# Performance work log

Measured on AMD Instinct MI355X. Metric: run time of the kernel, lower is better.

Reference implementation:

```python
import jax, jax.numpy as jnp
import numpy as np

NC, NK, K, PAD, SCALE, MID = 3, 64, 3, 1, 4, 4
K2, S2 = K * K, SCALE * SCALE
B, H, W = 4, 128, 128


def conv2d(x, w, b, pad):
    y = jax.lax.conv_general_dilated(x, w, (1, 1), [(pad, pad), (pad, pad)],
                                     dimension_numbers=('NCHW', 'OIHW', 'NCHW'))
    return y + b[None, :, None, None]


def bilinear_gather(x, py, px):
    # x: [B,C,H,W]; py/px: [B,K2,H,W] absolute (fractional) sample coords; zero outside.
    b, c, h, w = x.shape
    y0, x0 = jnp.floor(py), jnp.floor(px)
    wy, wx = py - y0, px - x0
    xf = x.reshape(b, c, h * w)

    def g(yi, xi):
        valid = ((yi >= 0) & (yi <= h - 1) & (xi >= 0) & (xi <= w - 1)).astype(x.dtype)
        yc = jnp.clip(yi, 0, h - 1).astype(jnp.int32)
        xc = jnp.clip(xi, 0, w - 1).astype(jnp.int32)
        idx = (yc * w + xc).reshape(b, -1)
        v = jax.vmap(lambda a, i: a[:, i])(xf, idx).reshape(b, c, *yi.shape[1:])
        return v * valid[:, None]

    return (((1 - wy) * (1 - wx))[:, None] * g(y0, x0)
            + ((1 - wy) * wx)[:, None] * g(y0, x0 + 1)
            + (wy * (1 - wx))[:, None] * g(y0 + 1, x0)
            + (wy * wx)[:, None] * g(y0 + 1, x0 + 1))


def deform_conv(x, ow, ob, mw, mb, w, b):
    # DCNv2: offsets [B,2*K2,H,W] (y,x interleaved per tap), modulation mask 2*sigmoid.
    bsz, c, h, ww = x.shape
    off = conv2d(x, ow, ob, PAD).reshape(bsz, K2, 2, h, ww)
    mask = 2.0 * jax.nn.sigmoid(conv2d(x, mw, mb, PAD))  # [B,K2,H,W]
    ky, kx = jnp.meshgrid(jnp.arange(K), jnp.arange(K), indexing='ij')
    py = jnp.arange(h)[None, None, :, None] + (ky.reshape(K2) - PAD)[None, :, None, None] + off[:, :, 0]
    px = jnp.arange(ww)[None, None, None, :] + (kx.reshape(K2) - PAD)[None, :, None, None] + off[:, :, 1]
    patches = bilinear_gather(x, py, px) * mask[:, None]  # [B,C,K2,H,W]
    return jnp.einsum('bckhw,ock->bohw', patches, w.reshape(w.shape[0], c, K2)) + b[None, :, None, None]


def convlstm(x, h, c, w, b):
    g = conv2d(jnp.concatenate([x, h], 1), w, b, PAD)
    i, f, o, gg = jnp.split(g, 4, axis=1)
    c = jax.nn.sigmoid(f) * c + jax.nn.sigmoid(i) * jnp.tanh(gg)
    return jax.nn.sigmoid(o) * jnp.tanh(c), c


def ddf_up(x, sp_w, sp_b, ch_w1, ch_b1, ch_w2, ch_b2):
    # DDFUpPack: S2 branches, per-pixel spatial filter + SE-style per-channel filter,
    # 'add' combine, per-branch dynamic KxK filtering, then pixel_shuffle(SCALE).
    bsz, c, h, w = x.shape
    sp = conv2d(x, sp_w.reshape(S2 * K2, c, K, K), sp_b.reshape(S2 * K2), PAD).reshape(bsz, S2, K2, h, w)
    pooled = x.mean((2, 3))  # global avg pool -> [B,C]
    h1 = jax.nn.relu(jnp.einsum('bc,smc->bsm', pooled, ch_w1) + ch_b1[None])
    ch = (jnp.einsum('bsm,skm->bsk', h1, ch_w2) + ch_b2[None]).reshape(bsz, S2, c, K2)
    xp = jnp.pad(x, ((0, 0), (0, 0), (PAD, PAD), (PAD, PAD)))
    patches = jnp.stack([xp[:, :, i:i + h, j:j + w] for i in range(K) for j in range(K)], 2)  # [B,C,K2,H,W]
    filt = ch[:, :, :, :, None, None] + sp[:, :, None]  # [B,S2,C,K2,H,W]
    out = jnp.einsum('bckhw,bsckhw->bcshw', patches, filt)  # [B,C,S2,H,W]
    out = out.reshape(bsz, c, SCALE, SCALE, h, w).transpose(0, 1, 4, 2, 5, 3)
    return out.reshape(bsz, c, h * SCALE, w * SCALE)  # pixel_shuffle


def _forward(X, lstm_w, lstm_b,
             d1_ow, d1_ob, d1_mw, d1_mb, d1_w, d1_b,
             d2_ow, d2_ob, d2_mw, d2_mb, d2_w, d2_b,
             d3_ow, d3_ob, d3_mw, d3_mb, d3_w, d3_b,
             conv_w, conv_b, sp_w, sp_b, ch_w1, ch_b1, ch_w2, ch_b2):
    lr = X
    bsz, _, h, w = X.shape
    z = jnp.zeros((bsz, NK, h, w), X.dtype)
    hid, cell = convlstm(X, z, z, lstm_w, lstm_b)
    x = deform_conv(jnp.concatenate([hid, lr], 1), d1_ow, d1_ob, d1_mw, d1_mb, d1_w, d1_b)
    x = deform_conv(jnp.concatenate([x, lr], 1), d2_ow, d2_ob, d2_mw, d2_mb, d2_w, d2_b)
    x = deform_conv(jnp.concatenate([x, lr], 1), d3_ow, d3_ob, d3_mw, d3_mb, d3_w, d3_b)
    x = conv2d(jnp.concatenate([x, lr], 1), conv_w, conv_b, PAD)
    out = jnp.clip(ddf_up(x, sp_w, sp_b, ch_w1, ch_b1, ch_w2, ch_b2), 0.0, 255.0)
    return out, hid, cell


def setup_inputs():
    key = jax.random.key(0)
    ks = iter(jax.random.split(key, 40))

    def p(shape, s=0.05):
        return jax.random.normal(next(ks), shape, jnp.float32) * s

    cin = NK + NC
    d = {'X': jax.random.normal(next(ks), (B, NC, H, W), jnp.float32),
         'lstm_w': p((4 * NK, NC + NK, K, K)), 'lstm_b': p((4 * NK,))}
    for i in (1, 2, 3):
        d[f'd{i}_ow'] = p((2 * K2, cin, K, K)); d[f'd{i}_ob'] = p((2 * K2,))
        d[f'd{i}_mw'] = p((K2, cin, K, K));     d[f'd{i}_mb'] = p((K2,))
        d[f'd{i}_w'] = p((NK, cin, K, K));      d[f'd{i}_b'] = p((NK,))
    d['conv_w'] = p((NC, cin, K, K)); d['conv_b'] = p((NC,))
    d['sp_w'] = p((S2, K2, NC, K, K)); d['sp_b'] = p((S2, K2))
    d['ch_w1'] = p((S2, MID, NC)); d['ch_b1'] = p((S2, MID))
    d['ch_w2'] = p((S2, NC * K2, MID)); d['ch_b2'] = p((S2, NC * K2))
    return d


def reference(X, lstm_w, lstm_b,
              d1_ow, d1_ob, d1_mw, d1_mb, d1_w, d1_b,
              d2_ow, d2_ob, d2_mw, d2_mb, d2_w, d2_b,
              d3_ow, d3_ob, d3_mw, d3_mb, d3_w, d3_b,
              conv_w, conv_b, sp_w, sp_b, ch_w1, ch_b1, ch_w2, ch_b2):
    return _forward(X, lstm_w, lstm_b,
                    d1_ow, d1_ob, d1_mw, d1_mb, d1_w, d1_b,
                    d2_ow, d2_ob, d2_mw, d2_mb, d2_w, d2_b,
                    d3_ow, d3_ob, d3_mw, d3_mb, d3_w, d3_b,
                    conv_w, conv_b, sp_w, sp_b, ch_w1, ch_b1, ch_w2, ch_b2)
```

## Files before the change

### kernel.cpp

```cpp
#include <hip/hip_runtime.h>
#include <hip/hip_bf16.h>
#include <math.h>

#define NC 3
#define NK 64
#define KK 3
#define K2 9
#define PAD 1
#define SCALE 4
#define S2 16
#define MID 4
#define B 4
#define H 128
#define W 128
#define HW (H*W)
#define CIN 67
#define OUT_HW (H*SCALE)
#define CST 64
#define NSTRIPE 64

typedef short bf16x8 __attribute__((ext_vector_type(8)));
typedef float f32x4 __attribute__((ext_vector_type(4)));
typedef float f32x2 __attribute__((ext_vector_type(2)));
typedef unsigned int u32x4 __attribute__((ext_vector_type(4)));
typedef unsigned int u32x2 __attribute__((ext_vector_type(2)));

__device__ __forceinline__ float fast_sigmoid(float v) { return 1.f / (1.f + __expf(-v)); }
__device__ __forceinline__ float fast_tanh(float v) { return 2.f / (1.f + __expf(-2.f * v)) - 1.f; }

__device__ __forceinline__ unsigned short f2bf(float f) {
    unsigned int u = __float_as_uint(f);
    unsigned int r = (u + 0x7FFFu + ((u >> 16) & 1u)) >> 16;
    return (unsigned short)r;
}

__device__ __forceinline__ f32x2 unpk(unsigned int u) {
    f32x2 r;
    r[0] = __uint_as_float(u << 16);
    r[1] = __uint_as_float(u & 0xffff0000u);
    return r;
}

__device__ __forceinline__ void load_patch(const float* __restrict__ xc, int y, int x, float* p) {
#pragma unroll
    for (int dy = -1; dy <= 1; dy++) {
#pragma unroll
        for (int dx = -1; dx <= 1; dx++) {
            int yy = y + dy, xx = x + dx;
            float v = (yy >= 0 && yy < H && xx >= 0 && xx < W) ? xc[yy * W + xx] : 0.f;
            p[(dy + 1) * 3 + (dx + 1)] = v;
        }
    }
}

__global__ void k_prep(const float* __restrict__ lw,
                       const float* __restrict__ dw0, const float* __restrict__ dw1,
                       const float* __restrict__ dw2,
                       const float* __restrict__ ow0, const float* __restrict__ ow1,
                       const float* __restrict__ ow2,
                       const float* __restrict__ mw0, const float* __restrict__ mw1,
                       const float* __restrict__ mw2,
                       unsigned short* __restrict__ aplk,
                       unsigned short* __restrict__ apk0, unsigned short* __restrict__ apk1,
                       unsigned short* __restrict__ apk2,
                       unsigned short* __restrict__ apkOM0, unsigned short* __restrict__ apkOM1,
                       unsigned short* __restrict__ apkOM2,
                       float* __restrict__ pooledS) {
    int g = blockIdx.x;
    int tid = threadIdx.x;
    int lane = tid >> 3, j = tid & 7;
    if (g == 0) { pooledS[tid] = 0.f; pooledS[tid + 512] = 0.f; }

    if (g < 12) {
        int o = g * 16 + (lane & 15);
        int k = ((lane >> 4) << 3) + j;
        float val = 0.f;
        if (k < 27) {
            int c = k / 9, tap = k % 9;
            int gate = o >> 6, nk = o & 63;
            int base = (gate == 0) ? 0 : (gate == 1) ? 2 * NK : 3 * NK;
            val = lw[(size_t)(base + nk) * (CIN * 9) + c * 9 + tap];
        }
        aplk[(size_t)g * 512 + tid] = f2bf(val);
    } else if (g < 336) {
        int gi = g - 12;
        int i = gi / 108, gg = gi - i * 108;
        const float* w = (i == 0) ? dw0 : (i == 1) ? dw1 : dw2;
        unsigned short* apk = (i == 0) ? apk0 : (i == 1) ? apk1 : apk2;
        int mt = gg & 3, r = gg >> 2;
        int ks = r % 3, tap = r / 3;
        int o = mt * 16 + (lane & 15);
        int c = ks * 32 + ((lane >> 4) << 3) + j;
        float val = (c < CIN) ? w[(size_t)o * (CIN * 9) + c * 9 + tap] : 0.f;
        apk[(size_t)gg * 512 + tid] = f2bf(val);
    } else {
        int gi = g - 336;
        int i = gi / 54, gg = gi - i * 54;
        const float* ow = (i == 0) ? ow0 : (i == 1) ? ow1 : ow2;
        const float* mw = (i == 0) ? mw0 : (i == 1) ? mw1 : mw2;
        unsigned short* apk = (i == 0) ? apkOM0 : (i == 1) ? apkOM1 : apkOM2;
        int mt = gg & 1, r = gg >> 1;
        int kss = r % 3, tap = r / 3;
        int o = mt * 16 + (lane & 15);
        int c = kss * 32 + ((lane >> 4) << 3) + j;
        float val = 0.f;
        if (c < CIN) {
            if (o < 18) val = ow[(size_t)o * (CIN * 9) + c * 9 + tap];
            else if (o < 27) val = mw[(size_t)(o - 18) * (CIN * 9) + c * 9 + tap];
        }
        apk[(size_t)gg * 512 + tid] = f2bf(val);
    }
}

__global__ __launch_bounds__(256, 4) void k_lstm(const float* __restrict__ X,
                                                 const unsigned short* __restrict__ aplk,
                                                 const float* __restrict__ lb,
                                                 unsigned short* __restrict__ xcatA,
                                                 float* __restrict__ hid_out,
                                                 float* __restrict__ cell_out,
                                                 float* __restrict__ lrp) {
    int tid = threadIdx.x;
    int lane = tid & 63;
    int nt = __builtin_amdgcn_readfirstlane(tid >> 6);
    int blk = blockIdx.x;
    int sg = (blk & 7) * 128 + (blk >> 3);
    int b = sg >> 8;
    int hwbase = (sg & 255) * 64;
    int n = lane & 15, q = lane >> 4;
    int hw = hwbase + nt * 16 + n;
    int y = hw >> 7, x = hw & (W - 1);

    if (nt == 0) {
        int px = hwbase + lane;
        f32x4 v = {X[(size_t)(b * NC + 0) * HW + px], X[(size_t)(b * NC + 1) * HW + px],
                   X[(size_t)(b * NC + 2) * HW + px], 0.f};
        *(f32x4*)(lrp + ((size_t)b * HW + px) * 4) = v;
    }

    bf16x8 bf;
#pragma unroll
    for (int j = 0; j < 8; j++) {
        int k = q * 8 + j;
        float v = 0.f;
        if (k < 27) {
            int c = k / 9, tap = k % 9;
            int ky = tap / 3, kx = tap % 3;
            int yy = y + ky - 1, xx = x + kx - 1;
            if (yy >= 0 && yy < H && xx >= 0 && xx < W)
                v = X[(size_t)(b * NC + c) * HW + yy * W + xx];
        }
        bf[j] = (short)f2bf(v);
    }

    f32x4 acc[12];
#pragma unroll
    for (int mt = 0; mt < 12; mt++) { f32x4 z = {0.f, 0.f, 0.f, 0.f}; acc[mt] = z; }
#pragma unroll
    for (int mt = 0; mt < 12; mt++) {
        bf16x8 af = *(const bf16x8*)(aplk + (size_t)mt * 512 + lane * 8);
        acc[mt] = __builtin_amdgcn_mfma_f32_16x16x32_bf16(af, bf, acc[mt], 0, 0, 0);
    }

    unsigned short* xo = xcatA + (size_t)b * HW * CST;
#pragma unroll
    for (int mt = 0; mt < 4; mt++) {
        float hv4[4];
#pragma unroll
        for (int r = 0; r < 4; r++) {
            int nk = mt * 16 + q * 4 + r;
            float gi = acc[mt][r] + lb[nk];
            float go = acc[mt + 4][r] + lb[2 * NK + nk];
            float gg = acc[mt + 8][r] + lb[3 * NK + nk];
            float cv = fast_sigmoid(gi) * fast_tanh(gg);
            float hv = fast_sigmoid(go) * fast_tanh(cv);
            hv4[r] = hv;
            hid_out[(size_t)(b * NK + nk) * HW + hw] = hv;
            cell_out[(size_t)(b * NK + nk) * HW + hw] = cv;
        }
        u32x2 st;
        st[0] = (unsigned int)f2bf(hv4[0]) | ((unsigned int)f2bf(hv4[1]) << 16);
        st[1] = (unsigned int)f2bf(hv4[2]) | ((unsigned int)f2bf(hv4[3]) << 16);
        int p = 2 * mt + (q >> 1);
        *(u32x2*)(xo + (((size_t)p * HW + hw) << 3) + (q & 1) * 4) = st;
    }
}

__global__ __launch_bounds__(256, 4) void k_offdef(const unsigned short* __restrict__ xcat,
                                                   const float* __restrict__ lrp,
                                                   const unsigned short* __restrict__ apkom,
                                                   const float* __restrict__ ob,
                                                   const float* __restrict__ mb,
                                                   const unsigned short* __restrict__ apk,
                                                   const float* __restrict__ bias,
                                                   unsigned short* __restrict__ xout) {
    __shared__ float somp[4][16][37];
    int tid = threadIdx.x;
    int lane = tid & 63;
    int wid = __builtin_amdgcn_readfirstlane(tid >> 6);
    int blk = blockIdx.x;
    int sg = (blk & 7) * 128 + (blk >> 3);
    int b = sg >> 8;
    int hwbase = (sg & 255) * 64;
    int n = lane & 15, q = lane >> 4;
    int hw = hwbase + wid * 16 + n;
    int y = hw >> 7, x = hw & (W - 1);

    const unsigned short* xb = xcat + (size_t)b * HW * CST;
    const unsigned short* pl0 = xb + (((size_t)q * HW) << 3);
    const unsigned short* pl1 = xb + (((size_t)(4 + q) * HW) << 3);
    const float* lb_ = lrp + (size_t)b * HW * 4;

    {
        f32x4 acc2[2];
#pragma unroll
        for (int mt = 0; mt < 2; mt++) { f32x4 z = {0.f, 0.f, 0.f, 0.f}; acc2[mt] = z; }
#pragma unroll
        for (int tap = 0; tap < K2; tap++) {
            int ky = tap / 3, kx = tap - ky * 3;
            int yy = y + ky - 1, xx = x + kx - 1;
            bool vld = (yy >= 0 && yy < H && xx >= 0 && xx < W);
            int ii = min(max(yy, 0), H - 1) * W + min(max(xx, 0), W - 1);
            const unsigned short* ab = apkom + (size_t)(tap * 6) * 512 + lane * 8;
            {
                bf16x8 bfv = *(const bf16x8*)(pl0 + ((size_t)ii << 3));
                if (!vld) { bf16x8 z = {0, 0, 0, 0, 0, 0, 0, 0}; bfv = z; }
#pragma unroll
                for (int mt = 0; mt < 2; mt++) {
                    bf16x8 af = *(const bf16x8*)(ab + (size_t)(0 * 2 + mt) * 512);
                    acc2[mt] = __builtin_amdgcn_mfma_f32_16x16x32_bf16(af, bfv, acc2[mt], 0, 0, 0);
                }
            }
            {
                bf16x8 bfv = *(const bf16x8*)(pl1 + ((size_t)ii << 3));
                if (!vld) { bf16x8 z = {0, 0, 0, 0, 0, 0, 0, 0}; bfv = z; }
#pragma unroll
                for (int mt = 0; mt < 2; mt++) {
                    bf16x8 af = *(const bf16x8*)(ab + (size_t)(1 * 2 + mt) * 512);
                    acc2[mt] = __builtin_amdgcn_mfma_f32_16x16x32_bf16(af, bfv, acc2[mt], 0, 0, 0);
                }
            }
            bf16x8 bf2 = {0, 0, 0, 0, 0, 0, 0, 0};
            if (q == 0 && vld) {
                f32x4 L = *(const f32x4*)(lb_ + ((size_t)ii << 2));
#pragma unroll
                for (int j = 0; j < 4; j++) bf2[j] = (short)f2bf(L[j]);
            }
#pragma unroll
            for (int mt = 0; mt < 2; mt++) {
                bf16x8 af = *(const bf16x8*)(ab + (size_t)(4 + mt) * 512);
                acc2[mt] = __builtin_amdgcn_mfma_f32_16x16x32_bf16(af, bf2, acc2[mt], 0, 0, 0);
            }
        }
#pragma unroll
        for (int mt = 0; mt < 2; mt++)
#pragma unroll
            for (int r = 0; r < 4; r++) {
                int o = mt * 16 + q * 4 + r;
                float s = acc2[mt][r];
                if (o < 18)
                    somp[wid][n][(o >> 1) * 4 + (o & 1)] = s + ob[o];
                else if (o < 27)
                    somp[wid][n][(o - 18) * 4 + 2] = 2.f * fast_sigmoid(s + mb[o - 18]);
            }
    }
    __syncthreads();

    f32x4 acc[4];
#pragma unroll
    for (int mt = 0; mt < 4; mt++) { f32x4 z = {0.f, 0.f, 0.f, 0.f}; acc[mt] = z; }

#pragma unroll
    for (int tap = 0; tap < K2; tap++) {
        float omy = somp[wid][n][tap * 4 + 0];
        float omx = somp[wid][n][tap * 4 + 1];
        float m = somp[wid][n][tap * 4 + 2];
        int ky = tap / 3, kx = tap - ky * 3;
        float py = (float)(y + ky - 1) + omy;
        float px_ = (float)(x + kx - 1) + omx;
        float fy = floorf(py), fx = floorf(px_);
        float wy = py - fy, wx = px_ - fx;
        int y0 = (int)fy, x0 = (int)fx;
        int y1 = y0 + 1, x1 = x0 + 1;
        float vy0 = (y0 >= 0 && y0 <= H - 1) ? 1.f : 0.f;
        float vy1 = (y1 >= 0 && y1 <= H - 1) ? 1.f : 0.f;
        float vx0 = (x0 >= 0 && x0 <= W - 1) ? 1.f : 0.f;
        float vx1 = (x1 >= 0 && x1 <= W - 1) ? 1.f : 0.f;
        int yc0 = min(max(y0, 0), H - 1), yc1 = min(max(y1, 0), H - 1);
        int xc0 = min(max(x0, 0), W - 1), xc1 = min(max(x1, 0), W - 1);
        float a00 = (1.f - wy) * (1.f - wx) * m * vy0 * vx0;
        float a01 = (1.f - wy) * wx * m * vy0 * vx1;
        float a10 = wy * (1.f - wx) * m * vy1 * vx0;
        float a11 = wy * wx * m * vy1 * vx1;
        int j00 = yc0 * W + xc0, j01 = yc0 * W + xc1;
        int j10 = yc1 * W + xc0, j11 = yc1 * W + xc1;

        const unsigned short* ab = apk + (size_t)(tap * 12) * 512 + lane * 8;
        {
            u32x4 d00 = *(const u32x4*)(pl0 + ((size_t)j00 << 3));
            u32x4 d01 = *(const u32x4*)(pl0 + ((size_t)j01 << 3));
            u32x4 d10 = *(const u32x4*)(pl0 + ((size_t)j10 << 3));
            u32x4 d11 = *(const u32x4*)(pl0 + ((size_t)j11 << 3));
            bf16x8 bf;
            unsigned int* bfu = (unsigned int*)&bf;
#pragma unroll
            for (int e = 0; e < 4; e++) {
                f32x2 v = unpk(d00[e]) * a00 + unpk(d01[e]) * a01
                        + unpk(d10[e]) * a10 + unpk(d11[e]) * a11;
                bfu[e] = (unsigned int)f2bf(v[0]) | ((unsigned int)f2bf(v[1]) << 16);
            }
#pragma unroll
            for (int mt = 0; mt < 4; mt++) {
                bf16x8 af = *(const bf16x8*)(ab + (size_t)(0 * 4 + mt) * 512);
                acc[mt] = __builtin_amdgcn_mfma_f32_16x16x32_bf16(af, bf, acc[mt], 0, 0, 0);
            }
        }
        {
            u32x4 d00 = *(const u32x4*)(pl1 + ((size_t)j00 << 3));
            u32x4 d01 = *(const u32x4*)(pl1 + ((size_t)j01 << 3));
            u32x4 d10 = *(const u32x4*)(pl1 + ((size_t)j10 << 3));
            u32x4 d11 = *(const u32x4*)(pl1 + ((size_t)j11 << 3));
            bf16x8 bf;
            unsigned int* bfu = (unsigned int*)&bf;
#pragma unroll
            for (int e = 0; e < 4; e++) {
                f32x2 v = unpk(d00[e]) * a00 + unpk(d01[e]) * a01
                        + unpk(d10[e]) * a10 + unpk(d11[e]) * a11;
                bfu[e] = (unsigned int)f2bf(v[0]) | ((unsigned int)f2bf(v[1]) << 16);
            }
#pragma unroll
            for (int mt = 0; mt < 4; mt++) {
                bf16x8 af = *(const bf16x8*)(ab + (size_t)(1 * 4 + mt) * 512);
                acc[mt] = __builtin_amdgcn_mfma_f32_16x16x32_bf16(af, bf, acc[mt], 0, 0, 0);
            }
        }
        bf16x8 bf2 = {0, 0, 0, 0, 0, 0, 0, 0};
        if (q == 0) {
            f32x4 L00 = *(const f32x4*)(lb_ + ((size_t)j00 << 2));
            f32x4 L01 = *(const f32x4*)(lb_ + ((size_t)j01 << 2));
            f32x4 L10 = *(const f32x4*)(lb_ + ((size_t)j10 << 2));
            f32x4 L11 = *(const f32x4*)(lb_ + ((size_t)j11 << 2));
            f32x4 Lv = L00 * a00 + L01 * a01 + L10 * a10 + L11 * a11;
#pragma unroll
            for (int j = 0; j < 4; j++) bf2[j] = (short)f2bf(Lv[j]);
        }
#pragma unroll
        for (int mt = 0; mt < 4; mt++) {
            bf16x8 af = *(const bf16x8*)(ab + (size_t)(2 * 4 + mt) * 512);
            acc[mt] = __builtin_amdgcn_mfma_f32_16x16x32_bf16(af, bf2, acc[mt], 0, 0, 0);
        }
    }

    unsigned short* xo = xout + (size_t)b * HW * CST;
#pragma unroll
    for (int mt = 0; mt < 4; mt++) {
        float s[4];
#pragma unroll
        for (int r = 0; r < 4; r++) {
            int o = mt * 16 + q * 4 + r;
            s[r] = acc[mt][r] + bias[o];
        }
        u32x2 st;
        st[0] = (unsigned int)f2bf(s[0]) | ((unsigned int)f2bf(s[1]) << 16);
        st[1] = (unsigned int)f2bf(s[2]) | ((unsigned int)f2bf(s[3]) << 16);
        int p = 2 * mt + (q >> 1);
        *(u32x2*)(xo + (((size_t)p * HW + hw) << 3) + (q & 1) * 4) = st;
    }
}

__global__ __launch_bounds__(256, 4) void k_conv3(const unsigned short* __restrict__ xcat,
                                                  const float* __restrict__ lrp,
                                                  const float* __restrict__ cw,
                                                  const float* __restrict__ cb,
                                                  float* __restrict__ y3,
                                                  float* __restrict__ pooledS) {
    __shared__ float red[4 * 3 * 64];
    __shared__ float s_cw[NC * CIN * 9];
    int tid = threadIdx.x;
    int lane = tid & 63;
    int wid = __builtin_amdgcn_readfirstlane(tid >> 6);
    int blk = blockIdx.x;
    int sg = (blk & 7) * 128 + (blk >> 3);
    int b = sg >> 8;
    int hwbase = (sg & 255) * 64;
    int hw = hwbase + lane;
    int y = hw >> 7, x = hw & (W - 1);
    int t0 = (wid == 0) ? 0 : 3 + (wid - 1) * 2;
    int t1 = (wid == 0) ? 3 : t0 + 2;

    for (int i = tid; i < NC * CIN * 9; i += 256) s_cw[i] = cw[i];
    __syncthreads();

    float a0 = 0.f, a1 = 0.f, a2 = 0.f;
    const unsigned short* xb = xcat + (size_t)b * HW * CST;
    const float* lb_ = lrp + (size_t)b * HW * 4;
#pragma unroll 1
    for (int tap = t0; tap < t1; tap++) {
        int ky = tap / 3, kx = tap - ky * 3;
        int yy = y + ky - 1, xx = x + kx - 1;
        if (yy < 0 || yy >= H || xx < 0 || xx >= W) continue;
        int ii = yy * W + xx;
#pragma unroll
        for (int c8 = 0; c8 < 8; c8++) {
            u32x4 d = *(const u32x4*)(xb + (((size_t)c8 * HW + ii) << 3));
#pragma unroll
            for (int e = 0; e < 4; e++) {
                int c = c8 * 8 + e * 2;
                float lo = __uint_as_float(d[e] << 16);
                float hi = __uint_as_float(d[e] & 0xffff0000u);
                a0 += lo * s_cw[0 * (CIN * 9) + c * 9 + tap] + hi * s_cw[0 * (CIN * 9) + (c + 1) * 9 + tap];
                a1 += lo * s_cw[1 * (CIN * 9) + c * 9 + tap] + hi * s_cw[1 * (CIN * 9) + (c + 1) * 9 + tap];
                a2 += lo * s_cw[2 * (CIN * 9) + c * 9 + tap] + hi * s_cw[2 * (CIN * 9) + (c + 1) * 9 + tap];
            }
        }
        f32x4 L = *(const f32x4*)(lb_ + ((size_t)ii << 2));
#pragma unroll
        for (int e = 0; e < 3; e++) {
            a0 += L[e] * s_cw[0 * (CIN * 9) + (64 + e) * 9 + tap];
            a1 += L[e] * s_cw[1 * (CIN * 9) + (64 + e) * 9 + tap];
            a2 += L[e] * s_cw[2 * (CIN * 9) + (64 + e) * 9 + tap];
        }
    }
    red[(wid * 3 + 0) * 64 + lane] = a0;
    red[(wid * 3 + 1) * 64 + lane] = a1;
    red[(wid * 3 + 2) * 64 + lane] = a2;
    __syncthreads();
    if (tid < 192) {
        int oc = tid >> 6, px = tid & 63;
        float s = red[(0 * 3 + oc) * 64 + px] + red[(1 * 3 + oc) * 64 + px]
                + red[(2 * 3 + oc) * 64 + px] + red[(3 * 3 + oc) * 64 + px];
        float v = s + cb[oc];
        y3[(size_t)(b * NC + oc) * HW + hwbase + px] = v;
        float r = v;
#pragma unroll
        for (int off = 32; off > 0; off >>= 1) r += __shfl_xor(r, off);
        if ((tid & 63) == 0)
            atomicAdd(&pooledS[(blk & (NSTRIPE - 1)) * 16 + b * NC + oc], r * (1.f / (float)HW));
    }
}

__global__ __launch_bounds__(256) void k_ddf(const float* __restrict__ y3,
                                             const float* __restrict__ spw,
                                             const float* __restrict__ spb,
                                             const float* __restrict__ pooledS,
                                             const float* __restrict__ ch_w1,
                                             const float* __restrict__ ch_b1,
                                             const float* __restrict__ ch_w2,
                                             const float* __restrict__ ch_b2,
                                             float* __restrict__ out) {
    __shared__ float s_spw[4 * K2 * NC * 9];
    __shared__ float s_spb[4 * K2];
    __shared__ float s_ch[4 * NC * K2];
    __shared__ float s_pool[NC];
    int t = blockIdx.x * blockDim.x + threadIdx.x;
    int b = t >> 14, hw = t & (HW - 1), y = hw >> 7, x = hw & (W - 1);
    int s0 = blockIdx.y * 4;
    for (int i = threadIdx.x; i < 4 * K2 * NC * 9; i += 256) s_spw[i] = spw[s0 * K2 * NC * 9 + i];
    if (threadIdx.x < 4 * K2) s_spb[threadIdx.x] = spb[s0 * K2 + threadIdx.x];
    if (threadIdx.x < NC) {
        float s = 0.f;
#pragma unroll
        for (int st = 0; st < NSTRIPE; st++) s += pooledS[st * 16 + b * NC + threadIdx.x];
        s_pool[threadIdx.x] = s;
    }
    __syncthreads();
    if (threadIdx.x < 4 * NC * K2) {
        int t2 = threadIdx.x;
        int si = t2 / (NC * K2), kk = t2 - si * (NC * K2);
        int s = s0 + si;
        float a = ch_b2[s * (NC * K2) + kk];
#pragma unroll
        for (int m = 0; m < MID; m++) {
            float h1 = ch_b1[s * MID + m];
#pragma unroll
            for (int c = 0; c < NC; c++) h1 += s_pool[c] * ch_w1[(s * MID + m) * NC + c];
            a += fmaxf(h1, 0.f) * ch_w2[(s * (NC * K2) + kk) * MID + m];
        }
        s_ch[t2] = a;
    }
    __syncthreads();
    float p[NC][9];
#pragma unroll
    for (int c = 0; c < NC; c++) load_patch(y3 + (b * NC + c) * HW, y, x, p[c]);
    f32x4 ov[NC];
#pragma unroll
    for (int si = 0; si < 4; si++) {
        float spv[K2];
#pragma unroll
        for (int k = 0; k < K2; k++) {
            float a = s_spb[si * K2 + k];
            const float* w = s_spw + (si * K2 + k) * (NC * 9);
#pragma unroll
            for (int c = 0; c < NC; c++)
#pragma unroll
                for (int tt = 0; tt < 9; tt++) a += p[c][tt] * w[c * 9 + tt];
            spv[k] = a;
        }
#pragma unroll
        for (int c = 0; c < NC; c++) {
            float a = 0.f;
            const float* chp = s_ch + (si * NC + c) * K2;
#pragma unroll
            for (int k = 0; k < K2; k++) a += p[c][k] * (chp[k] + spv[k]);
            ov[c][si] = fminf(fmaxf(a, 0.f), 255.f);
        }
    }
    int sy = s0 >> 2;
#pragma unroll
    for (int c = 0; c < NC; c++)
        *(f32x4*)(out + ((size_t)(b * NC + c) * OUT_HW + (y * SCALE + sy)) * OUT_HW + x * SCALE) = ov[c];
}

extern "C" void kernel_launch(void* const* d_in, const int* in_sizes, int n_in,
                              void* d_out, int out_size, void* d_ws, size_t ws_size,
                              hipStream_t stream) {
    const float* X = (const float*)d_in[0];
    const float* lstm_w = (const float*)d_in[1];
    const float* lstm_b = (const float*)d_in[2];
    const float* ow[3] = {(const float*)d_in[3], (const float*)d_in[9], (const float*)d_in[15]};
    const float* ob[3] = {(const float*)d_in[4], (const float*)d_in[10], (const float*)d_in[16]};
    const float* mw[3] = {(const float*)d_in[5], (const float*)d_in[11], (const float*)d_in[17]};
    const float* mb[3] = {(const float*)d_in[6], (const float*)d_in[12], (const float*)d_in[18]};
    const float* dw[3] = {(const float*)d_in[7], (const float*)d_in[13], (const float*)d_in[19]};
    const float* db[3] = {(const float*)d_in[8], (const float*)d_in[14], (const float*)d_in[20]};
    const float* conv_w = (const float*)d_in[21];
    const float* conv_b = (const float*)d_in[22];
    const float* sp_w = (const float*)d_in[23];
    const float* sp_b = (const float*)d_in[24];
    const float* ch_w1 = (const float*)d_in[25];
    const float* ch_b1 = (const float*)d_in[26];
    const float* ch_w2 = (const float*)d_in[27];
    const float* ch_b2 = (const float*)d_in[28];

    float* out = (float*)d_out;
    const size_t OUT_IMG = (size_t)B * NC * OUT_HW * OUT_HW;
    const size_t HIDSZ = (size_t)B * NK * HW;
    float* hid_out = out + OUT_IMG;
    float* cell_out = out + OUT_IMG + HIDSZ;

    float* ws = (float*)d_ws;
    const size_t XCATF = (size_t)B * HW * CST / 2;
    unsigned short* xcatA = (unsigned short*)ws;  ws += XCATF;
    unsigned short* xcatB = (unsigned short*)ws;  ws += XCATF;
    float* lrp = ws;              ws += (size_t)B * HW * 4;
    unsigned short* apk[3];
    for (int i = 0; i < 3; i++) { apk[i] = (unsigned short*)ws; ws += 108 * 512 / 2; }
    unsigned short* apkOM[3];
    for (int i = 0; i < 3; i++) { apkOM[i] = (unsigned short*)ws; ws += 54 * 512 / 2; }
    unsigned short* aplk = (unsigned short*)ws;  ws += 12 * 512 / 2;
    float* y3 = ws;               ws += (size_t)B * NC * HW;
    float* pooledS = ws;          ws += NSTRIPE * 16;

    dim3 blk(256);
    dim3 g4(B * HW / 256, 4);
    dim3 gd(B * HW / 64);

    k_prep<<<dim3(498), dim3(512), 0, stream>>>(
        lstm_w, dw[0], dw[1], dw[2], ow[0], ow[1], ow[2], mw[0], mw[1], mw[2],
        aplk, apk[0], apk[1], apk[2], apkOM[0], apkOM[1], apkOM[2], pooledS);

    k_lstm<<<gd, blk, 0, stream>>>(X, aplk, lstm_b, xcatA, hid_out, cell_out, lrp);

    k_offdef<<<gd, blk, 0, stream>>>(xcatA, lrp, apkOM[0], ob[0], mb[0], apk[0], db[0], xcatB);
    k_offdef<<<gd, blk, 0, stream>>>(xcatB, lrp, apkOM[1], ob[1], mb[1], apk[1], db[1], xcatA);
    k_offdef<<<gd, blk, 0, stream>>>(xcatA, lrp, apkOM[2], ob[2], mb[2], apk[2], db[2], xcatB);

    k_conv3<<<gd, blk, 0, stream>>>(xcatB, lrp, conv_w, conv_b, y3, pooledS);
    k_ddf<<<g4, blk, 0, stream>>>(y3, sp_w, sp_b, pooledS, ch_w1, ch_b1, ch_w2, ch_b2, out);
}
```

Measured before the change: 307.9 us.

## Split deform-conv taps across wave pairs with LDS reduction in k_offdef

Each block now covers 32 pixels instead of 64. The four waves are arranged as two pixel tiles times two tap halves: one half takes taps 0-4 and the other taps 5-8, for both the offset/mask conv and the deformable gather-MMA. Partial accumulators are summed through a new shared-memory buffer, which costs two extra barriers. The aim is to double the block count and shorten each wave's serial tap chain so gather latency is better hidden, at the price of LDS traffic and synchronisation. The launch bound is raised to 8 blocks per CU, which may force register spills.

```diff
diff --git a/kernel.cpp b/kernel.cpp
--- a/kernel.cpp
+++ b/kernel.cpp
@@ -185,7 +185,7 @@
     }
 }
 
-__global__ __launch_bounds__(256, 4) void k_offdef(const unsigned short* __restrict__ xcat,
+__global__ __launch_bounds__(256, 8) void k_offdef(const unsigned short* __restrict__ xcat,
                                                    const float* __restrict__ lrp,
                                                    const unsigned short* __restrict__ apkom,
                                                    const float* __restrict__ ob,
@@ -193,16 +193,18 @@
                                                    const unsigned short* __restrict__ apk,
                                                    const float* __restrict__ bias,
                                                    unsigned short* __restrict__ xout) {
-    __shared__ float somp[4][16][37];
+    __shared__ float red[2 * 64 * 17];
+    __shared__ float somp[2][16][37];
     int tid = threadIdx.x;
     int lane = tid & 63;
     int wid = __builtin_amdgcn_readfirstlane(tid >> 6);
+    int nt2 = wid & 1, kh = wid >> 1;
     int blk = blockIdx.x;
-    int sg = (blk & 7) * 128 + (blk >> 3);
-    int b = sg >> 8;
-    int hwbase = (sg & 255) * 64;
+    int sg = (blk & 7) * 256 + (blk >> 3);
+    int b = sg >> 9;
+    int hwbase = (sg & 511) * 32;
     int n = lane & 15, q = lane >> 4;
-    int hw = hwbase + wid * 16 + n;
+    int hw = hwbase + nt2 * 16 + n;
     int y = hw >> 7, x = hw & (W - 1);
 
     const unsigned short* xb = xcat + (size_t)b * HW * CST;
@@ -214,8 +216,10 @@
         f32x4 acc2[2];
 #pragma unroll
         for (int mt = 0; mt < 2; mt++) { f32x4 z = {0.f, 0.f, 0.f, 0.f}; acc2[mt] = z; }
+        int c0_ = kh ? 0 : 5, c1_ = kh ? 5 : 9;
 #pragma unroll
         for (int tap = 0; tap < K2; tap++) {
+            if (tap < c0_ || tap >= c1_) continue;
             int ky = tap / 3, kx = tap - ky * 3;
             int yy = y + ky - 1, xx = x + kx - 1;
             bool vld = (yy >= 0 && yy < H && xx >= 0 && xx < W);
@@ -256,11 +260,22 @@
 #pragma unroll
             for (int r = 0; r < 4; r++) {
                 int o = mt * 16 + q * 4 + r;
-                float s = acc2[mt][r];
+                red[((nt2 * 2 + kh) * 32 + o) * 17 + n] = acc2[mt][r];
+            }
+    }
+    __syncthreads();
+    if (!kh) {
+#pragma unroll
+        for (int mt = 0; mt < 2; mt++)
+#pragma unroll
+            for (int r = 0; r < 4; r++) {
+                int o = mt * 16 + q * 4 + r;
+                float s = red[((nt2 * 2 + 0) * 32 + o) * 17 + n]
+                        + red[((nt2 * 2 + 1) * 32 + o) * 17 + n];
                 if (o < 18)
-                    somp[wid][n][(o >> 1) * 4 + (o & 1)] = s + ob[o];
+                    somp[nt2][n][(o >> 1) * 4 + (o & 1)] = s + ob[o];
                 else if (o < 27)
-                    somp[wid][n][(o - 18) * 4 + 2] = 2.f * fast_sigmoid(s + mb[o - 18]);
+                    somp[nt2][n][(o - 18) * 4 + 2] = 2.f * fast_sigmoid(s + mb[o - 18]);
             }
     }
     __syncthreads();
@@ -269,11 +284,13 @@
 #pragma unroll
     for (int mt = 0; mt < 4; mt++) { f32x4 z = {0.f, 0.f, 0.f, 0.f}; acc[mt] = z; }
 
+    int t0 = kh ? 5 : 0, t1 = kh ? 9 : 5;
 #pragma unroll
     for (int tap = 0; tap < K2; tap++) {
-        float omy = somp[wid][n][tap * 4 + 0];
-        float omx = somp[wid][n][tap * 4 + 1];
-        float m = somp[wid][n][tap * 4 + 2];
+        if (tap < t0 || tap >= t1) continue;
+        float omy = somp[nt2][n][tap * 4 + 0];
+        float omx = somp[nt2][n][tap * 4 + 1];
+        float m = somp[nt2][n][tap * 4 + 2];
         int ky = tap / 3, kx = tap - ky * 3;
         float py = (float)(y + ky - 1) + omy;
         float px_ = (float)(x + kx - 1) + omx;
@@ -350,20 +367,33 @@
         }
     }
 
-    unsigned short* xo = xout + (size_t)b * HW * CST;
-#pragma unroll
-    for (int mt = 0; mt < 4; mt++) {
-        float s[4];
-#pragma unroll
-        for (int r = 0; r < 4; r++) {
-            int o = mt * 16 + q * 4 + r;
-            s[r] = acc[mt][r] + bias[o];
-        }
-        u32x2 st;
-        st[0] = (unsigned int)f2bf(s[0]) | ((unsigned int)f2bf(s[1]) << 16);
-        st[1] = (unsigned int)f2bf(s[2]) | ((unsigned int)f2bf(s[3]) << 16);
-        int p = 2 * mt + (q >> 1);
-        *(u32x2*)(xo + (((size_t)p * HW + hw) << 3) + (q & 1) * 4) = st;
+    if (kh) {
+#pragma unroll
+        for (int mt = 0; mt < 4; mt++) {
+#pragma unroll
+            for (int r = 0; r < 4; r++) {
+                int o = mt * 16 + q * 4 + r;
+                red[(nt2 * 64 + o) * 17 + n] = acc[mt][r];
+            }
+        }
+    }
+    __syncthreads();
+    if (!kh) {
+        unsigned short* xo = xout + (size_t)b * HW * CST;
+#pragma unroll
+        for (int mt = 0; mt < 4; mt++) {
+            float s[4];
+#pragma unroll
+            for (int r = 0; r < 4; r++) {
+                int o = mt * 16 + q * 4 + r;
+                s[r] = acc[mt][r] + red[(nt2 * 64 + o) * 17 + n] + bias[o];
+            }
+            u32x2 st;
+            st[0] = (unsigned int)f2bf(s[0]) | ((unsigned int)f2bf(s[1]) << 16);
+            st[1] = (unsigned int)f2bf(s[2]) | ((unsigned int)f2bf(s[3]) << 16);
+            int p = 2 * mt + (q >> 1);
+            *(u32x2*)(xo + (((size_t)p * HW + hw) << 3) + (q & 1) * 4) = st;
+        }
     }
 }
 
@@ -553,6 +583,7 @@
     dim3 blk(256);
     dim3 g4(B * HW / 256, 4);
     dim3 gd(B * HW / 64);
+    dim3 gd2(B * HW / 32);
 
     k_prep<<<dim3(498), dim3(512), 0, stream>>>(
         lstm_w, dw[0], dw[1], dw[2], ow[0], ow[1], ow[2], mw[0], mw[1], mw[2],
@@ -560,9 +591,9 @@
 
     k_lstm<<<gd, blk, 0, stream>>>(X, aplk, lstm_b, xcatA, hid_out, cell_out, lrp);
 
-    k_offdef<<<gd, blk, 0, stream>>>(xcatA, lrp, apkOM[0], ob[0], mb[0], apk[0], db[0], xcatB);
-    k_offdef<<<gd, blk, 0, stream>>>(xcatB, lrp, apkOM[1], ob[1], mb[1], apk[1], db[1], xcatA);
-    k_offdef<<<gd, blk, 0, stream>>>(xcatA, lrp, apkOM[2], ob[2], mb[2], apk[2], db[2], xcatB);
+    k_offdef<<<gd2, blk, 0, stream>>>(xcatA, lrp, apkOM[0], ob[0], mb[0], apk[0], db[0], xcatB);
+    k_offdef<<<gd2, blk, 0, stream>>>(xcatB, lrp, apkOM[1], ob[1], mb[1], apk[1], db[1], xcatA);
+    k_offdef<<<gd2, blk, 0, stream>>>(xcatA, lrp, apkOM[2], ob[2], mb[2], apk[2], db[2], xcatB);
 
     k_conv3<<<gd, blk, 0, stream>>>(xcatB, lrp, conv_w, conv_b, y3, pooledS);
     k_ddf<<<g4, blk, 0, stream>>>(y3, sp_w, sp_b, pooledS, ch_w1, ch_b1, ch_w2, ch_b2, out);
```

Measured after the change: 366.2 us. 19.0% more time.
